# Performance work log

Measured on AMD Instinct MI355X. Metric: run time of the kernel, lower is better.

## Reference

```python
import jax, jax.numpy as jnp
import numpy as np

EMBED = 8      # embed_dim == n_qubits == d_k (forced by reshapes in the source)
FFN = 2048
LN_EPS = 1e-5


def _layernorm(x, g, b):
    mu = jnp.mean(x, axis=-1, keepdims=True)
    var = jnp.mean(jnp.square(x - mu), axis=-1, keepdims=True)
    return (x - mu) * jax.lax.rsqrt(var + LN_EPS) * g + b


def _quantum_measure(theta):
    # RX(theta_i) on each wire of |0..0>, CNOT ladder 0->1->...->n-1,
    # then <Z_i>. Closed form: <Z_i> = prod_{j<=i} cos(theta_j).
    return jnp.cumprod(jnp.cos(theta), axis=-1)


def setup_inputs() -> dict:
    key = jax.random.key(0)
    ks = jax.random.split(key, 8)
    B, S = 32, 4096
    s_e = 1.0 / np.sqrt(EMBED)
    s_f = 1.0 / np.sqrt(FFN)
    return {
        "x": jax.random.normal(ks[0], (B, S, EMBED), jnp.float32),
        "Wq": jax.random.uniform(ks[1], (EMBED, EMBED), jnp.float32, -s_e, s_e),
        "Wo": jax.random.uniform(ks[2], (EMBED, EMBED), jnp.float32, -s_e, s_e),
        "W1": jax.random.uniform(ks[3], (FFN, EMBED), jnp.float32, -s_e, s_e),
        "b1": jax.random.uniform(ks[4], (FFN,), jnp.float32, -s_e, s_e),
        "W2": jax.random.uniform(ks[5], (EMBED, FFN), jnp.float32, -s_f, s_f),
        "b2": jax.random.uniform(ks[6], (EMBED,), jnp.float32, -s_f, s_f),
        "g1": jnp.ones((EMBED,), jnp.float32),
        "beta1": jnp.zeros((EMBED,), jnp.float32),
        "g2": jnp.ones((EMBED,), jnp.float32),
        "beta2": jnp.zeros((EMBED,), jnp.float32),
    }


def reference(x, Wq, Wo, W1, b1, W2, b2, g1, beta1, g2, beta2):
    # Quantum multi-head attention (num_heads=1, d_k=n_wires=8).
    # Note: k_proj / v_proj outputs are unused in the original forward.
    q = jnp.einsum("bse,fe->bsf", x, Wq)          # (B,S,E)
    attn = jnp.einsum("bse,fe->bsf", _quantum_measure(q), Wo)
    h = _layernorm(x + attn, g1, beta1)           # dropout is identity (eval)
    # Quantum feed-forward: measure -> linear1 -> relu -> linear2
    m = _quantum_measure(h)                       # (B,S,E)
    hid = jax.nn.relu(jnp.einsum("bse,fe->bsf", m, W1) + b1)  # (B,S,FFN)
    ffn = jnp.einsum("bsf,ef->bse", hid, W2) + b2
    return _layernorm(h + ffn, g2, beta2)
```

## Files before the change

kernel.cpp:

```cpp
#include <hip/hip_runtime.h>
#include <hip/hip_bf16.h>

#define FFN 2048
#define LN_EPS 1e-5f

typedef __attribute__((ext_vector_type(8))) short bf16x8;
typedef __attribute__((ext_vector_type(4))) short bf16x4;
typedef __attribute__((ext_vector_type(4))) float f32x4;

union FragU  { bf16x8 v; unsigned u[4]; uint4 q; };
union Frag2U { bf16x4 v; unsigned u[2]; uint2 d; };

static __device__ __forceinline__ unsigned cvtpk(float lo, float hi) {
    unsigned r;
    asm("v_cvt_pk_bf16_f32 %0, %1, %2" : "=v"(r) : "v"(lo), "v"(hi));
    return r;
}

static __device__ __forceinline__ ushort to_bf16(float f) {
    unsigned u = __float_as_uint(f);
    u += 0x7fffu + ((u >> 16) & 1u);
    return (ushort)(u >> 16);
}
static __device__ __forceinline__ float frombf(ushort u) {
    return __uint_as_float((unsigned)u << 16);
}
static __device__ __forceinline__ unsigned pk2u(ushort a, ushort b) {
    return (unsigned)a | ((unsigned)b << 16);
}

__global__ __launch_bounds__(256) void tbq_prep(
    const float* __restrict__ W1, const float* __restrict__ b1,
    const float* __restrict__ W2, uint4* __restrict__ ws)
{
    const int b = blockIdx.x;
    if (b < 34) {
        const int idx = b * 256 + threadIdx.x;
        if (idx < 2112) {
            const int rec = idx / 33, r = idx % 33;
            ushort v[8] = {0,0,0,0,0,0,0,0};
            if (r) {
                const int l32 = r - 1, g = l32 >> 3, c = l32 & 7, cc = rec;
                #pragma unroll
                for (int j = 0; j < 8; ++j) {
                    const int fl = 4 * g + (j & 3) + 16 * (j >> 2);
                    v[j] = to_bf16(0.5f * W2[c * FFN + cc * 32 + fl]);
                }
            }
            union { ushort s[8]; uint4 q; } pk;
            #pragma unroll
            for (int j = 0; j < 8; ++j) pk.s[j] = v[j];
            ws[idx] = pk.q;
        } else if (idx < 8512) {
            const int i2 = idx - 2112;
            const int rec = i2 / 50, r = i2 % 50;
            const int s = rec & 1, cc = rec >> 1;
            uint2 val = make_uint2(0u, 0u);
            if (r >= 1 && r <= 32) {
                const int l32 = r - 1, c = l32 & 15, gg = l32 >> 4;
                const int f = cc * 32 + s * 16 + c;
                val.x = pk2u(to_bf16(W1[f * 8 + 4 * gg + 0]), to_bf16(W1[f * 8 + 4 * gg + 1]));
                val.y = pk2u(to_bf16(W1[f * 8 + 4 * gg + 2]), to_bf16(W1[f * 8 + 4 * gg + 3]));
            } else if (r >= 33 && r <= 48) {
                const int c = r - 33;
                const int f = cc * 32 + s * 16 + c;
                val.x = pk2u(to_bf16(b1[f]), 0);
            }
            ((uint2*)ws)[4224 + i2] = val;
        }
    } else {
        const int w = (b - 34) * 4 + (threadIdx.x >> 6);
        const int lane = threadIdx.x & 63;
        const int e = w / 9, k = w % 9;
        float acc = 0.0f;
        #pragma unroll 4
        for (int i = 0; i < 32; ++i) {
            const int f = lane + i * 64;
            const float w2v = frombf(to_bf16(0.5f * W2[e * FFN + f]));
            const float ov  = (k < 8) ? frombf(to_bf16(W1[f * 8 + k]))
                                      : frombf(to_bf16(b1[f]));
            acc += w2v * ov;
        }
        #pragma unroll
        for (int m = 32; m >= 1; m >>= 1) acc += __shfl_xor(acc, m, 64);
        if (lane == 0) ((float*)ws)[21248 + w] = acc;
    }
}

#define TB_A(ACC, F0V, F1V, A2V, B1V)                                                  \
    asm volatile(                                                                      \
        "v_mfma_f32_16x16x16_bf16 v[40:43], %[f0], %[b1], %[z]\n\t"                    \
        "v_mfma_f32_16x16x16_bf16 v[44:47], %[f1], %[b1], %[z]\n\t"                    \
        "s_nop 7\n\t"                                                                  \
        "s_nop 7\n\t"                                                                  \
        "v_cvt_pk_bf16_f32 v48, |v40|, |v41|\n\t"                                      \
        "v_cvt_pk_bf16_f32 v49, |v42|, |v43|\n\t"                                      \
        "v_cvt_pk_bf16_f32 v50, |v44|, |v45|\n\t"                                      \
        "v_cvt_pk_bf16_f32 v51, |v46|, |v47|\n\t"                                      \
        "s_nop 3\n\t"                                                                  \
        "v_mfma_f32_16x16x32_bf16 %[acc], %[a2], v[48:51], %[acc]"                     \
        : [acc] "+v"(ACC)                                                              \
        : [f0] "v"(F0V), [f1] "v"(F1V), [a2] "v"(A2V), [b1] "v"(B1V), [z] "v"(z4)      \
        : "v40","v41","v42","v43","v44","v45","v46","v47","v48","v49","v50","v51")

#define TB_B(ACC, F0V, F1V, A2V, B1V)                                                  \
    asm volatile(                                                                      \
        "v_mfma_f32_16x16x16_bf16 v[52:55], %[f0], %[b1], %[z]\n\t"                    \
        "v_mfma_f32_16x16x16_bf16 v[56:59], %[f1], %[b1], %[z]\n\t"                    \
        "s_nop 7\n\t"                                                                  \
        "s_nop 7\n\t"                                                                  \
        "v_cvt_pk_bf16_f32 v60, |v52|, |v53|\n\t"                                      \
        "v_cvt_pk_bf16_f32 v61, |v54|, |v55|\n\t"                                      \
        "v_cvt_pk_bf16_f32 v62, |v56|, |v57|\n\t"                                      \
        "v_cvt_pk_bf16_f32 v63, |v58|, |v59|\n\t"                                      \
        "s_nop 3\n\t"                                                                  \
        "v_mfma_f32_16x16x32_bf16 %[acc], %[a2], v[60:63], %[acc]"                     \
        : [acc] "+v"(ACC)                                                              \
        : [f0] "v"(F0V), [f1] "v"(F1V), [a2] "v"(A2V), [b1] "v"(B1V), [z] "v"(z4)      \
        : "v52","v53","v54","v55","v56","v57","v58","v59","v60","v61","v62","v63")

__global__ __launch_bounds__(256) void tbq_mfma(
    const float* __restrict__ x,
    const float* __restrict__ Wq,
    const float* __restrict__ Wo,
    const float* __restrict__ b2,
    const float* __restrict__ g1,
    const float* __restrict__ beta1,
    const float* __restrict__ g2,
    const float* __restrict__ beta2,
    const uint4* __restrict__ ws,
    float* __restrict__ out)
{
    __shared__ __align__(16) uint4 mS[128];
    __shared__ __align__(16) float part[4][128][8];

    const int tid  = threadIdx.x;
    const int lane = tid & 63;
    const int wv   = tid >> 6;
    const int c    = lane & 15;
    const int g    = lane >> 4;
    const int tok0 = blockIdx.x * 128;

    const uint2* ws2 = (const uint2*)ws;
    const float* M   = (const float*)ws + 21248;

    const int o1x = (g < 2) ? (1 + c + 16 * g) : ((g == 2) ? (33 + c) : 0);
    const int o2  = ((lane & 8) == 0) ? (1 + ((lane >> 4) << 3) + (lane & 7)) : 0;
    const int cc0 = wv * 16;

    Frag2U F0[4], F1[4];
    FragU  A2[4];
    #pragma unroll
    for (int p = 0; p < 3; ++p) {
        const int cc = cc0 + p;
        F0[p].d = ws2[4224 + (cc * 2 + 0) * 50 + o1x];
        F1[p].d = ws2[4224 + (cc * 2 + 1) * 50 + o1x];
        A2[p].q = (ws + cc * 33)[o2];
    }

    float h[8], m[8];
    if (tid < 128) {
        const int t = tok0 + tid;
        const float4* xr = (const float4*)(x + (size_t)t * 8);
        float4 xa = xr[0], xb = xr[1];
        float xv[8] = {xa.x, xa.y, xa.z, xa.w, xb.x, xb.y, xb.z, xb.w};

        float qm[8];
        {
            float cp = 1.0f;
            #pragma unroll
            for (int f = 0; f < 8; ++f) {
                float acc = 0.0f;
                #pragma unroll
                for (int e = 0; e < 8; ++e) acc += xv[e] * Wq[f * 8 + e];
                cp *= __cosf(acc);
                qm[f] = cp;
            }
        }
        float mu = 0.0f;
        #pragma unroll
        for (int f = 0; f < 8; ++f) {
            float acc = 0.0f;
            #pragma unroll
            for (int e = 0; e < 8; ++e) acc += qm[e] * Wo[f * 8 + e];
            h[f] = xv[f] + acc;
            mu += h[f];
        }
        mu *= 0.125f;
        float var = 0.0f;
        #pragma unroll
        for (int i = 0; i < 8; ++i) { float d = h[i] - mu; var += d * d; }
        var *= 0.125f;
        float rs = rsqrtf(var + LN_EPS);
        #pragma unroll
        for (int i = 0; i < 8; ++i) h[i] = (h[i] - mu) * rs * g1[i] + beta1[i];

        {
            float cp = 1.0f;
            #pragma unroll
            for (int i = 0; i < 8; ++i) { cp *= __cosf(h[i]); m[i] = cp; }
        }
        uint4 mq;
        mq.x = cvtpk(m[0], m[1]); mq.y = cvtpk(m[2], m[3]);
        mq.z = cvtpk(m[4], m[5]); mq.w = cvtpk(m[6], m[7]);
        mS[tid] = mq;
    }
    __syncthreads();

    Frag2U B1[8];
    #pragma unroll
    for (int T = 0; T < 8; ++T) {
        uint4 mr = mS[T * 16 + c];
        unsigned u0 = (g == 0) ? mr.x : ((g == 1) ? mr.z : ((g == 2) ? 0x00003F80u : 0u));
        unsigned u1 = (g == 0) ? mr.y : ((g == 1) ? mr.w : 0u);
        B1[T].u[0] = u0;
        B1[T].u[1] = u1;
    }

    f32x4 z4 = {0.f, 0.f, 0.f, 0.f};
    asm volatile("" : "+v"(z4));

    f32x4 acc[8] = {{0,0,0,0},{0,0,0,0},{0,0,0,0},{0,0,0,0},
                    {0,0,0,0},{0,0,0,0},{0,0,0,0},{0,0,0,0}};
    asm volatile("s_nop 3" ::: "memory");

    #pragma unroll
    for (int i = 0; i < 16; ++i) {
        const int cur = i & 3;
        if (i + 3 < 16) {
            const int ns = (i + 3) & 3;
            const int cc = cc0 + i + 3;
            F0[ns].d = ws2[4224 + (cc * 2 + 0) * 50 + o1x];
            F1[ns].d = ws2[4224 + (cc * 2 + 1) * 50 + o1x];
            A2[ns].q = (ws + cc * 33)[o2];
        }
        __builtin_amdgcn_s_setprio(1);
        TB_A(acc[0], F0[cur].v, F1[cur].v, A2[cur].v, B1[0].v);
        TB_B(acc[1], F0[cur].v, F1[cur].v, A2[cur].v, B1[1].v);
        TB_A(acc[2], F0[cur].v, F1[cur].v, A2[cur].v, B1[2].v);
        TB_B(acc[3], F0[cur].v, F1[cur].v, A2[cur].v, B1[3].v);
        TB_A(acc[4], F0[cur].v, F1[cur].v, A2[cur].v, B1[4].v);
        TB_B(acc[5], F0[cur].v, F1[cur].v, A2[cur].v, B1[5].v);
        TB_A(acc[6], F0[cur].v, F1[cur].v, A2[cur].v, B1[6].v);
        TB_B(acc[7], F0[cur].v, F1[cur].v, A2[cur].v, B1[7].v);
        __builtin_amdgcn_s_setprio(0);
    }
    asm volatile("s_nop 7\n\ts_nop 7" ::: "memory");

    if (g < 2) {
        #pragma unroll
        for (int T = 0; T < 8; ++T) {
            *(f32x4*)&part[wv][T * 16 + c][4 * g] = acc[T];
        }
    }
    __syncthreads();

    if (tid < 128) {
        float mb[9];
        #pragma unroll
        for (int k = 0; k < 8; ++k) mb[k] = frombf(to_bf16(m[k]));
        mb[8] = 1.0f;

        float ffnv[8];
        #pragma unroll
        for (int e = 0; e < 8; ++e) {
            float s = part[0][tid][e] + part[1][tid][e]
                    + part[2][tid][e] + part[3][tid][e];
            float lin = 0.0f;
            #pragma unroll
            for (int k = 0; k < 9; ++k) lin += M[e * 9 + k] * mb[k];
            ffnv[e] = s + lin;
        }

        float o[8];
        float mu2 = 0.0f;
        #pragma unroll
        for (int i = 0; i < 8; ++i) { o[i] = h[i] + ffnv[i] + b2[i]; mu2 += o[i]; }
        mu2 *= 0.125f;
        float v2 = 0.0f;
        #pragma unroll
        for (int i = 0; i < 8; ++i) { float d = o[i] - mu2; v2 += d * d; }
        v2 *= 0.125f;
        float rs2 = rsqrtf(v2 + LN_EPS);

        float res[8];
        #pragma unroll
        for (int i = 0; i < 8; ++i) res[i] = (o[i] - mu2) * rs2 * g2[i] + beta2[i];

        float4* orow = (float4*)(out + (size_t)(tok0 + tid) * 8);
        orow[0] = make_float4(res[0], res[1], res[2], res[3]);
        orow[1] = make_float4(res[4], res[5], res[6], res[7]);
    }
}

extern "C" void kernel_launch(void* const* d_in, const int* in_sizes, int n_in,
                              void* d_out, int out_size, void* d_ws, size_t ws_size,
                              hipStream_t stream) {
    const float* x     = (const float*)d_in[0];
    const float* Wq    = (const float*)d_in[1];
    const float* Wo    = (const float*)d_in[2];
    const float* W1    = (const float*)d_in[3];
    const float* b1    = (const float*)d_in[4];
    const float* W2    = (const float*)d_in[5];
    const float* b2    = (const float*)d_in[6];
    const float* g1    = (const float*)d_in[7];
    const float* beta1 = (const float*)d_in[8];
    const float* g2    = (const float*)d_in[9];
    const float* beta2 = (const float*)d_in[10];
    float* out = (float*)d_out;
    uint4* ws = (uint4*)d_ws;

    tbq_prep<<<52, 256, 0, stream>>>(W1, b1, W2, ws);

    const int ntok = in_sizes[0] / 8;
    const int grid = ntok / 128;
    tbq_mfma<<<grid, 256, 0, stream>>>(x, Wq, Wo, b2, g1, beta1, g2, beta2, ws, out);
}
```

Before: 34.95 us.

## Split per-token attention/LN1 into pre-kernel and shrink MFMA blocks to 32 tokens

The per-token query projection, cosine cumprod, output projection and first layernorm move out of the MFMA kernel into the prep launch. That launch writes the bf16-packed measurements to workspace and the normalized h into the output buffer. The MFMA kernel then processes 32 tokens per block instead of 128, with an occupancy hint of 8 and no software prefetch ring. This is meant to raise the number of resident waves and drop the serial per-token prologue and LDS staging from the FFN kernel. In exchange it adds a global round trip for h and m, more repeated weight-fragment loads per token, and less in-wave MFMA independence.

```diff
diff --git a/kernel.cpp b/kernel.cpp
--- a/kernel.cpp
+++ b/kernel.cpp
@@ -16,7 +16,6 @@
     asm("v_cvt_pk_bf16_f32 %0, %1, %2" : "=v"(r) : "v"(lo), "v"(hi));
     return r;
 }
-
 static __device__ __forceinline__ ushort to_bf16(float f) {
     unsigned u = __float_as_uint(f);
     u += 0x7fffu + ((u >> 16) & 1u);
@@ -29,9 +28,17 @@
     return (unsigned)a | ((unsigned)b << 16);
 }
 
-__global__ __launch_bounds__(256) void tbq_prep(
+#define M_BASE 5400
+
+__global__ __launch_bounds__(256) void tbq_pre(
+    const float* __restrict__ x,
+    const float* __restrict__ Wq,
+    const float* __restrict__ Wo,
+    const float* __restrict__ g1,
+    const float* __restrict__ beta1,
     const float* __restrict__ W1, const float* __restrict__ b1,
-    const float* __restrict__ W2, uint4* __restrict__ ws)
+    const float* __restrict__ W2,
+    uint4* __restrict__ ws, float* __restrict__ hout)
 {
     const int b = blockIdx.x;
     if (b < 34) {
@@ -68,7 +75,7 @@
             }
             ((uint2*)ws)[4224 + i2] = val;
         }
-    } else {
+    } else if (b < 52) {
         const int w = (b - 34) * 4 + (threadIdx.x >> 6);
         const int lane = threadIdx.x & 63;
         const int e = w / 9, k = w % 9;
@@ -84,10 +91,61 @@
         #pragma unroll
         for (int m = 32; m >= 1; m >>= 1) acc += __shfl_xor(acc, m, 64);
         if (lane == 0) ((float*)ws)[21248 + w] = acc;
-    }
-}
-
-#define TB_A(ACC, F0V, F1V, A2V, B1V)                                                  \
+    } else {
+        const int t = (b - 52) * 256 + threadIdx.x;
+        const float4* xr = (const float4*)(x + (size_t)t * 8);
+        float4 xa = xr[0], xb = xr[1];
+        float xv[8] = {xa.x, xa.y, xa.z, xa.w, xb.x, xb.y, xb.z, xb.w};
+
+        float qm[8];
+        {
+            float cp = 1.0f;
+            #pragma unroll
+            for (int f = 0; f < 8; ++f) {
+                float acc = 0.0f;
+                #pragma unroll
+                for (int e = 0; e < 8; ++e) acc += xv[e] * Wq[f * 8 + e];
+                cp *= __cosf(acc);
+                qm[f] = cp;
+            }
+        }
+        float h[8];
+        float mu = 0.0f;
+        #pragma unroll
+        for (int f = 0; f < 8; ++f) {
+            float acc = 0.0f;
+            #pragma unroll
+            for (int e = 0; e < 8; ++e) acc += qm[e] * Wo[f * 8 + e];
+            h[f] = xv[f] + acc;
+            mu += h[f];
+        }
+        mu *= 0.125f;
+        float var = 0.0f;
+        #pragma unroll
+        for (int i = 0; i < 8; ++i) { float d = h[i] - mu; var += d * d; }
+        var *= 0.125f;
+        float rs = rsqrtf(var + LN_EPS);
+        #pragma unroll
+        for (int i = 0; i < 8; ++i) h[i] = (h[i] - mu) * rs * g1[i] + beta1[i];
+
+        float m[8];
+        {
+            float cp = 1.0f;
+            #pragma unroll
+            for (int i = 0; i < 8; ++i) { cp *= __cosf(h[i]); m[i] = cp; }
+        }
+        uint4 mq;
+        mq.x = cvtpk(m[0], m[1]); mq.y = cvtpk(m[2], m[3]);
+        mq.z = cvtpk(m[4], m[5]); mq.w = cvtpk(m[6], m[7]);
+        ws[M_BASE + t] = mq;
+
+        float4* hr = (float4*)(hout + (size_t)t * 8);
+        hr[0] = make_float4(h[0], h[1], h[2], h[3]);
+        hr[1] = make_float4(h[4], h[5], h[6], h[7]);
+    }
+}
+
+#define TB(ACC, F0V, F1V, A2V, B1V)                                                    \
     asm volatile(                                                                      \
         "v_mfma_f32_16x16x16_bf16 v[40:43], %[f0], %[b1], %[z]\n\t"                    \
         "v_mfma_f32_16x16x16_bf16 v[44:47], %[f1], %[b1], %[z]\n\t"                    \
@@ -103,163 +161,78 @@
         : [f0] "v"(F0V), [f1] "v"(F1V), [a2] "v"(A2V), [b1] "v"(B1V), [z] "v"(z4)      \
         : "v40","v41","v42","v43","v44","v45","v46","v47","v48","v49","v50","v51")
 
-#define TB_B(ACC, F0V, F1V, A2V, B1V)                                                  \
-    asm volatile(                                                                      \
-        "v_mfma_f32_16x16x16_bf16 v[52:55], %[f0], %[b1], %[z]\n\t"                    \
-        "v_mfma_f32_16x16x16_bf16 v[56:59], %[f1], %[b1], %[z]\n\t"                    \
-        "s_nop 7\n\t"                                                                  \
-        "s_nop 7\n\t"                                                                  \
-        "v_cvt_pk_bf16_f32 v60, |v52|, |v53|\n\t"                                      \
-        "v_cvt_pk_bf16_f32 v61, |v54|, |v55|\n\t"                                      \
-        "v_cvt_pk_bf16_f32 v62, |v56|, |v57|\n\t"                                      \
-        "v_cvt_pk_bf16_f32 v63, |v58|, |v59|\n\t"                                      \
-        "s_nop 3\n\t"                                                                  \
-        "v_mfma_f32_16x16x32_bf16 %[acc], %[a2], v[60:63], %[acc]"                     \
-        : [acc] "+v"(ACC)                                                              \
-        : [f0] "v"(F0V), [f1] "v"(F1V), [a2] "v"(A2V), [b1] "v"(B1V), [z] "v"(z4)      \
-        : "v52","v53","v54","v55","v56","v57","v58","v59","v60","v61","v62","v63")
-
-__global__ __launch_bounds__(256) void tbq_mfma(
-    const float* __restrict__ x,
-    const float* __restrict__ Wq,
-    const float* __restrict__ Wo,
+__global__ __launch_bounds__(256, 8) void tbq_mfma(
     const float* __restrict__ b2,
-    const float* __restrict__ g1,
-    const float* __restrict__ beta1,
     const float* __restrict__ g2,
     const float* __restrict__ beta2,
     const uint4* __restrict__ ws,
     float* __restrict__ out)
 {
-    __shared__ __align__(16) uint4 mS[128];
-    __shared__ __align__(16) float part[4][128][8];
+    __shared__ __align__(16) float part[4][32][8];
 
     const int tid  = threadIdx.x;
     const int lane = tid & 63;
     const int wv   = tid >> 6;
     const int c    = lane & 15;
     const int g    = lane >> 4;
-    const int tok0 = blockIdx.x * 128;
+    const int tok0 = blockIdx.x * 32;
 
     const uint2* ws2 = (const uint2*)ws;
-    const float* M   = (const float*)ws + 21248;
 
     const int o1x = (g < 2) ? (1 + c + 16 * g) : ((g == 2) ? (33 + c) : 0);
     const int o2  = ((lane & 8) == 0) ? (1 + ((lane >> 4) << 3) + (lane & 7)) : 0;
     const int cc0 = wv * 16;
 
-    Frag2U F0[4], F1[4];
-    FragU  A2[4];
+    Frag2U B1[2];
     #pragma unroll
-    for (int p = 0; p < 3; ++p) {
-        const int cc = cc0 + p;
-        F0[p].d = ws2[4224 + (cc * 2 + 0) * 50 + o1x];
-        F1[p].d = ws2[4224 + (cc * 2 + 1) * 50 + o1x];
-        A2[p].q = (ws + cc * 33)[o2];
-    }
-
-    float h[8], m[8];
-    if (tid < 128) {
-        const int t = tok0 + tid;
-        const float4* xr = (const float4*)(x + (size_t)t * 8);
-        float4 xa = xr[0], xb = xr[1];
-        float xv[8] = {xa.x, xa.y, xa.z, xa.w, xb.x, xb.y, xb.z, xb.w};
-
-        float qm[8];
-        {
-            float cp = 1.0f;
-            #pragma unroll
-            for (int f = 0; f < 8; ++f) {
-                float acc = 0.0f;
-                #pragma unroll
-                for (int e = 0; e < 8; ++e) acc += xv[e] * Wq[f * 8 + e];
-                cp *= __cosf(acc);
-                qm[f] = cp;
-            }
-        }
-        float mu = 0.0f;
-        #pragma unroll
-        for (int f = 0; f < 8; ++f) {
-            float acc = 0.0f;
-            #pragma unroll
-            for (int e = 0; e < 8; ++e) acc += qm[e] * Wo[f * 8 + e];
-            h[f] = xv[f] + acc;
-            mu += h[f];
-        }
-        mu *= 0.125f;
-        float var = 0.0f;
-        #pragma unroll
-        for (int i = 0; i < 8; ++i) { float d = h[i] - mu; var += d * d; }
-        var *= 0.125f;
-        float rs = rsqrtf(var + LN_EPS);
-        #pragma unroll
-        for (int i = 0; i < 8; ++i) h[i] = (h[i] - mu) * rs * g1[i] + beta1[i];
-
-        {
-            float cp = 1.0f;
-            #pragma unroll
-            for (int i = 0; i < 8; ++i) { cp *= __cosf(h[i]); m[i] = cp; }
-        }
-        uint4 mq;
-        mq.x = cvtpk(m[0], m[1]); mq.y = cvtpk(m[2], m[3]);
-        mq.z = cvtpk(m[4], m[5]); mq.w = cvtpk(m[6], m[7]);
-        mS[tid] = mq;
-    }
-    __syncthreads();
-
-    Frag2U B1[8];
-    #pragma unroll
-    for (int T = 0; T < 8; ++T) {
-        uint4 mr = mS[T * 16 + c];
-        unsigned u0 = (g == 0) ? mr.x : ((g == 1) ? mr.z : ((g == 2) ? 0x00003F80u : 0u));
-        unsigned u1 = (g == 0) ? mr.y : ((g == 1) ? mr.w : 0u);
-        B1[T].u[0] = u0;
-        B1[T].u[1] = u1;
+    for (int T = 0; T < 2; ++T) {
+        uint4 mr = ws[M_BASE + tok0 + T * 16 + c];
+        B1[T].u[0] = (g == 0) ? mr.x : ((g == 1) ? mr.z : ((g == 2) ? 0x00003F80u : 0u));
+        B1[T].u[1] = (g == 0) ? mr.y : ((g == 1) ? mr.w : 0u);
     }
 
     f32x4 z4 = {0.f, 0.f, 0.f, 0.f};
     asm volatile("" : "+v"(z4));
 
-    f32x4 acc[8] = {{0,0,0,0},{0,0,0,0},{0,0,0,0},{0,0,0,0},
-                    {0,0,0,0},{0,0,0,0},{0,0,0,0},{0,0,0,0}};
+    f32x4 acc0 = {0.f, 0.f, 0.f, 0.f};
+    f32x4 acc1 = {0.f, 0.f, 0.f, 0.f};
     asm volatile("s_nop 3" ::: "memory");
 
-    #pragma unroll
     for (int i = 0; i < 16; ++i) {
-        const int cur = i & 3;
-        if (i + 3 < 16) {
-            const int ns = (i + 3) & 3;
-            const int cc = cc0 + i + 3;
-            F0[ns].d = ws2[4224 + (cc * 2 + 0) * 50 + o1x];
-            F1[ns].d = ws2[4224 + (cc * 2 + 1) * 50 + o1x];
-            A2[ns].q = (ws + cc * 33)[o2];
-        }
+        const int cc = cc0 + i;
+        Frag2U F0, F1;
+        FragU  A2;
+        F0.d = ws2[4224 + (cc * 2 + 0) * 50 + o1x];
+        F1.d = ws2[4224 + (cc * 2 + 1) * 50 + o1x];
+        A2.q = (ws + cc * 33)[o2];
         __builtin_amdgcn_s_setprio(1);
-        TB_A(acc[0], F0[cur].v, F1[cur].v, A2[cur].v, B1[0].v);
-        TB_B(acc[1], F0[cur].v, F1[cur].v, A2[cur].v, B1[1].v);
-        TB_A(acc[2], F0[cur].v, F1[cur].v, A2[cur].v, B1[2].v);
-        TB_B(acc[3], F0[cur].v, F1[cur].v, A2[cur].v, B1[3].v);
-        TB_A(acc[4], F0[cur].v, F1[cur].v, A2[cur].v, B1[4].v);
-        TB_B(acc[5], F0[cur].v, F1[cur].v, A2[cur].v, B1[5].v);
-        TB_A(acc[6], F0[cur].v, F1[cur].v, A2[cur].v, B1[6].v);
-        TB_B(acc[7], F0[cur].v, F1[cur].v, A2[cur].v, B1[7].v);
+        TB(acc0, F0.v, F1.v, A2.v, B1[0].v);
+        TB(acc1, F0.v, F1.v, A2.v, B1[1].v);
         __builtin_amdgcn_s_setprio(0);
     }
     asm volatile("s_nop 7\n\ts_nop 7" ::: "memory");
 
     if (g < 2) {
-        #pragma unroll
-        for (int T = 0; T < 8; ++T) {
-            *(f32x4*)&part[wv][T * 16 + c][4 * g] = acc[T];
-        }
+        *(f32x4*)&part[wv][c][4 * g]      = acc0;
+        *(f32x4*)&part[wv][16 + c][4 * g] = acc1;
     }
     __syncthreads();
 
-    if (tid < 128) {
+    if (tid < 32) {
+        const int t = tok0 + tid;
+        const float* M = (const float*)ws + 21248;
+
+        uint4 mr = ws[M_BASE + t];
         float mb[9];
-        #pragma unroll
-        for (int k = 0; k < 8; ++k) mb[k] = frombf(to_bf16(m[k]));
+        mb[0] = frombf((ushort)(mr.x & 0xffff)); mb[1] = frombf((ushort)(mr.x >> 16));
+        mb[2] = frombf((ushort)(mr.y & 0xffff)); mb[3] = frombf((ushort)(mr.y >> 16));
+        mb[4] = frombf((ushort)(mr.z & 0xffff)); mb[5] = frombf((ushort)(mr.z >> 16));
+        mb[6] = frombf((ushort)(mr.w & 0xffff)); mb[7] = frombf((ushort)(mr.w >> 16));
         mb[8] = 1.0f;
+
+        const float4* hr = (const float4*)(out + (size_t)t * 8);
+        float4 ha = hr[0], hb = hr[1];
+        float h[8] = {ha.x, ha.y, ha.z, ha.w, hb.x, hb.y, hb.z, hb.w};
 
         float ffnv[8];
         #pragma unroll
@@ -287,7 +260,7 @@
         #pragma unroll
         for (int i = 0; i < 8; ++i) res[i] = (o[i] - mu2) * rs2 * g2[i] + beta2[i];
 
-        float4* orow = (float4*)(out + (size_t)(tok0 + tid) * 8);
+        float4* orow = (float4*)(out + (size_t)t * 8);
         orow[0] = make_float4(res[0], res[1], res[2], res[3]);
         orow[1] = make_float4(res[4], res[5], res[6], res[7]);
     }
@@ -310,9 +283,9 @@
     float* out = (float*)d_out;
     uint4* ws = (uint4*)d_ws;
 
-    tbq_prep<<<52, 256, 0, stream>>>(W1, b1, W2, ws);
-
     const int ntok = in_sizes[0] / 8;
-    const int grid = ntok / 128;
-    tbq_mfma<<<grid, 256, 0, stream>>>(x, Wq, Wo, b2, g1, beta1, g2, beta2, ws, out);
-}
+
+    tbq_pre<<<52 + ntok / 256, 256, 0, stream>>>(x, Wq, Wo, g1, beta1, W1, b1, W2, ws, out);
+
+    tbq_mfma<<<ntok / 32, 256, 0, stream>>>(b2, g2, beta2, ws, out);
+}
```

Measured after the change: 45.79 us. 31.0% more time.
